# Kernel optimization log

Hardware: AMD Instinct MI355X
Metric: run time of the kernel (lower is better)

The kernel has to match this reference:

```python
import jax, jax.numpy as jnp
import numpy as np

THETA_BINS = 8
PHI_BINS = 8
BLOCK_SIZE = 15  # odd, per assert
STRIDE = 1       # with stride=1, nr_block along each axis == image dim
EPS = 2.220446049250313e-16  # sys.float_info.epsilon, as in the original


def setup_inputs() -> dict:
    key = jax.random.key(0)
    x = jax.random.normal(key, (96, 96, 96), dtype=jnp.float32)
    return {"x": x}


def _sliding_sum0(a, bs):
    """Sliding-window sum of size bs along axis 0, stride 1, nblocks = a.shape[0].
    Windows extending past the end see zeros (original code indexes past the image;
    we treat out-of-range voxels as zero contribution)."""
    pad = [(0, bs - 1)] + [(0, 0)] * (a.ndim - 1)
    cs = jnp.cumsum(jnp.pad(a, pad), axis=0)
    cs = jnp.concatenate([jnp.zeros_like(cs[:1]), cs], axis=0)  # exclusive prefix
    return cs[bs:] - cs[:-bs]  # out[i] = sum a[i:i+bs]


def reference(x):
    Z, Y, X = x.shape
    Tb, Pb, BS = THETA_BINS, PHI_BINS, BLOCK_SIZE
    B = Tb * Pb

    # conv3d with fixed central-difference kernels, padding=1 (zero pad)
    p = jnp.pad(x, 1)
    gz = p[2:, 1:-1, 1:-1] - p[:-2, 1:-1, 1:-1]
    gy = p[1:-1, 2:, 1:-1] - p[1:-1, :-2, 1:-1]
    gx = p[1:-1, 1:-1, 2:] - p[1:-1, 1:-1, :-2]

    r = jnp.sqrt(gx * gx + gy * gy + gz * gz)
    theta = jnp.arctan(gy / (gx + EPS))          # range (-pi/2, pi/2)
    phi = jnp.arccos(gz / (r + EPS))             # range [0, pi]

    two_pi = jnp.float32(2.0 * np.pi)
    theta = jnp.where(theta < 0, theta + two_pi, theta)  # angle_normalizer(theta,0,2pi)

    t_raw = theta / (two_pi / Tb)
    p_raw = phi / (jnp.float32(np.pi) / Pb)

    lt = jnp.floor(t_raw).astype(jnp.int32)
    lt = jnp.where(lt == Tb, 0, lt)
    lp = jnp.floor(p_raw).astype(jnp.int32)
    lp = jnp.where(lp == Pb, 0, lp)
    ht = (lt + 1) % Tb
    hp = (lp + 1) % Pb

    # NOTE: the original uses the THETA fractional part for the phi ratios too
    # (a bug in the source) - reproduced faithfully here.
    frac = t_raw - jnp.floor(t_raw)
    w_lo = jnp.minimum(frac, 1.0 - frac)   # low-bin ratio per the branchy original
    w_hi = 1.0 - w_lo                      # high-bin ratio
    wp_lo = jnp.where(frac == 0, jnp.float32(1.0), w_lo)  # frac==0 -> phi not split
    wp_hi = 1.0 - wp_lo

    # per-voxel soft-binned histogram volume [N, B] via 4 scatter-adds
    n = r.size
    rows = jnp.arange(n)
    rf = r.reshape(-1)
    ltf, htf = lt.reshape(-1), ht.reshape(-1)
    lpf, hpf = lp.reshape(-1), hp.reshape(-1)
    wlof, whif = w_lo.reshape(-1), w_hi.reshape(-1)
    wplof, wphif = wp_lo.reshape(-1), wp_hi.reshape(-1)

    V = jnp.zeros((n, B), dtype=r.dtype)
    V = V.at[rows, ltf * Pb + lpf].add(rf * wlof * wplof)
    V = V.at[rows, htf * Pb + lpf].add(rf * whif * wplof)
    V = V.at[rows, ltf * Pb + hpf].add(rf * wlof * wphif)
    V = V.at[rows, htf * Pb + hpf].add(rf * whif * wphif)
    V = V.reshape(Z, Y, X, B)

    # block histograms: separable sliding-window sum over block_size^3, stride 1
    for ax in (0, 1, 2):
        V = jnp.moveaxis(_sliding_sum0(jnp.moveaxis(V, ax, 0), BS), 0, ax)

    return V[None, None]  # [1, 1, nbz, nby, nbx, theta_bins*phi_bins]
```

## Files before the change

kernel.cpp:

```cpp
#include <hip/hip_runtime.h>

typedef _Float16 half_t;
typedef __attribute__((ext_vector_type(8))) _Float16 half8;
typedef __attribute__((ext_vector_type(4))) _Float16 half4;

#define DIM 96
#define NBINS 64
#define BSZ 15
#define PADROWS (DIM + BSZ - 1)
#define NTHREADS 256
#define RS_F 68
#define RS4_F 17
#define RS_H 72
#define TY 4
#define YTILES (DIM / TY)

__device__ __forceinline__ void bin_line_scatter(
    const float* __restrict__ in, float* __restrict__ V,
    const int y, const int z, const int tid, const float sgn)
{
    if (tid < DIM) {
        const int x = tid;
        const int idx = (z * DIM + y) * DIM + x;
        const float xm = (x > 0)       ? in[idx - 1]         : 0.0f;
        const float xp = (x < DIM - 1) ? in[idx + 1]         : 0.0f;
        const float ym = (y > 0)       ? in[idx - DIM]       : 0.0f;
        const float yp = (y < DIM - 1) ? in[idx + DIM]       : 0.0f;
        const float zm = (z > 0)       ? in[idx - DIM * DIM] : 0.0f;
        const float zp = (z < DIM - 1) ? in[idx + DIM * DIM] : 0.0f;
        const float gx = xp - xm, gy = yp - ym, gz = zp - zm;

        const float EPSF  = 2.220446049250313e-16f;
        const float TWOPI = 6.28318530717958647692f;
        const float PIF   = 3.14159265358979323846f;

        const float r = sqrtf(gx * gx + gy * gy + gz * gz);
        float theta = atanf(gy / (gx + EPSF));
        const float phi = acosf(gz / (r + EPSF));
        if (theta < 0.0f) theta += TWOPI;
        const float t_raw = theta / (TWOPI / 8.0f);
        const float p_raw = phi   / (PIF   / 8.0f);
        const float ft = floorf(t_raw);
        const float fp = floorf(p_raw);
        int lt = (int)ft; if (lt == 8) lt = 0;
        int lp = (int)fp; if (lp == 8) lp = 0;
        const int ht = (lt + 1) & 7;
        const int hp = (lp + 1) & 7;
        const float frac  = t_raw - ft;
        const float w_lo  = fminf(frac, 1.0f - frac);
        const float w_hi  = 1.0f - w_lo;
        const float wp_lo = (frac == 0.0f) ? 1.0f : w_lo;
        const float wp_hi = 1.0f - wp_lo;

        const float rs = r * sgn;
        float* vrow = V + x * RS_F;
        vrow[lt * 8 + lp] += rs * w_lo * wp_lo;
        vrow[ht * 8 + lp] += rs * w_hi * wp_lo;
        vrow[lt * 8 + hp] += rs * w_lo * wp_hi;
        vrow[ht * 8 + hp] += rs * w_hi * wp_hi;
    }
}

__global__ __launch_bounds__(NTHREADS) void kA_bin_xy_h(
    const float* __restrict__ in, half_t* __restrict__ ws1)
{
    __shared__ float V[PADROWS * RS_F];
    const int tid = threadIdx.x;
    const int y0 = blockIdx.x * TY;
    const int z  = blockIdx.y;

    for (int i = tid; i < PADROWS * RS4_F; i += NTHREADS)
        ((float4*)V)[i] = make_float4(0.f, 0.f, 0.f, 0.f);
    __syncthreads();

    #pragma unroll
    for (int j = 0; j < BSZ - 1; ++j) {
        const int ys = y0 + j;
        if (ys < DIM) bin_line_scatter(in, V, ys, z, tid, 1.0f);
    }

    const int c8 = tid & 7;
    const int strip = tid >> 3;
    const int pos0 = strip * 3;
    const float4* V4 = (const float4*)V;

    for (int r = 0; r < TY; ++r) {
        const int y = y0 + r;
        if (y + BSZ - 1 < DIM) bin_line_scatter(in, V, y + BSZ - 1, z, tid, 1.0f);
        __syncthreads();

        float acc[8];
        #pragma unroll
        for (int k = 0; k < 8; ++k) acc[k] = 0.f;
        #pragma unroll
        for (int d = 0; d < BSZ; ++d) {
            const float4 a = V4[(pos0 + d) * RS4_F + c8 * 2];
            const float4 b = V4[(pos0 + d) * RS4_F + c8 * 2 + 1];
            acc[0] += a.x; acc[1] += a.y; acc[2] += a.z; acc[3] += a.w;
            acc[4] += b.x; acc[5] += b.y; acc[6] += b.z; acc[7] += b.w;
        }
        int pos = pos0;
        #pragma unroll
        for (int j = 0; j < 3; ++j) {
            half8 o;
            #pragma unroll
            for (int k = 0; k < 8; ++k) o[k] = (half_t)acc[k];
            *(half8*)(ws1 + (((size_t)(z * DIM + y) * DIM + pos) * NBINS + c8 * 8)) = o;
            if (j < 2) {
                const float4 a0 = V4[pos * RS4_F + c8 * 2];
                const float4 b0 = V4[pos * RS4_F + c8 * 2 + 1];
                const float4 a1 = V4[(pos + BSZ) * RS4_F + c8 * 2];
                const float4 b1 = V4[(pos + BSZ) * RS4_F + c8 * 2 + 1];
                acc[0] += a1.x - a0.x; acc[1] += a1.y - a0.y;
                acc[2] += a1.z - a0.z; acc[3] += a1.w - a0.w;
                acc[4] += b1.x - b0.x; acc[5] += b1.y - b0.y;
                acc[6] += b1.z - b0.z; acc[7] += b1.w - b0.w;
                ++pos;
            }
        }
        __syncthreads();
        if (r < TY - 1)
            bin_line_scatter(in, V, y, z, tid, -1.0f);
    }
}

__global__ __launch_bounds__(NTHREADS) void k3_zsum_h(
    const half_t* __restrict__ ws2, float* __restrict__ out)
{
    __shared__ half_t H[PADROWS * RS_H];
    const int tid = threadIdx.x;
    const int x = blockIdx.x, y = blockIdx.y;

    for (int i = tid; i < DIM * 8; i += NTHREADS) {
        const int pos = i >> 3, c8 = i & 7;
        *(half8*)&H[pos * RS_H + c8 * 8] =
            *(const half8*)(ws2 + (((size_t)(pos * DIM + y) * DIM + x) * NBINS + c8 * 8));
    }
    for (int i = tid; i < (PADROWS - DIM) * 8; i += NTHREADS) {
        const int pos = DIM + (i >> 3), c8 = i & 7;
        half8 zv = {};
        *(half8*)&H[pos * RS_H + c8 * 8] = zv;
    }
    __syncthreads();

    const int c4 = tid & 15;
    const int strip = tid >> 4;
    int pos = strip * 6;

    float4 s = make_float4(0.f, 0.f, 0.f, 0.f);
    #pragma unroll
    for (int d = 0; d < BSZ; ++d) {
        const half4 hv = *(const half4*)&H[(pos + d) * RS_H + c4 * 4];
        s.x += (float)hv[0]; s.y += (float)hv[1];
        s.z += (float)hv[2]; s.w += (float)hv[3];
    }
    float4* out4 = (float4*)out;
    #pragma unroll
    for (int j = 0; j < 6; ++j) {
        out4[((size_t)(pos * DIM + y) * DIM + x) * 16 + c4] = s;
        if (j < 5) {
            const half4 hs = *(const half4*)&H[pos * RS_H + c4 * 4];
            const half4 ha = *(const half4*)&H[(pos + BSZ) * RS_H + c4 * 4];
            s.x += (float)ha[0] - (float)hs[0]; s.y += (float)ha[1] - (float)hs[1];
            s.z += (float)ha[2] - (float)hs[2]; s.w += (float)ha[3] - (float)hs[3];
            ++pos;
        }
    }
}

__global__ __launch_bounds__(NTHREADS) void k1_bin_xsum_f(
    const float* __restrict__ in, float* __restrict__ out)
{
    __shared__ float V[PADROWS * RS_F];
    const int tid = threadIdx.x;
    const int y = blockIdx.x, z = blockIdx.y;

    for (int i = tid; i < PADROWS * RS4_F; i += NTHREADS)
        ((float4*)V)[i] = make_float4(0.f, 0.f, 0.f, 0.f);
    __syncthreads();
    bin_line_scatter(in, V, y, z, tid, 1.0f);
    __syncthreads();

    const int c4 = tid & 15;
    const int strip = tid >> 4;
    int pos = strip * 6;
    const float4* V4 = (const float4*)V;

    float4 s = make_float4(0.f, 0.f, 0.f, 0.f);
    #pragma unroll
    for (int d = 0; d < BSZ; ++d) {
        const float4 v = V4[(pos + d) * RS4_F + c4];
        s.x += v.x; s.y += v.y; s.z += v.z; s.w += v.w;
    }
    float4* out4 = (float4*)out;
    const int base = (z * DIM + y) * DIM * 16;
    out4[base + pos * 16 + c4] = s;
    #pragma unroll
    for (int j = 1; j < 6; ++j) {
        const float4 a = V4[pos * RS4_F + c4];
        const float4 b = V4[(pos + BSZ) * RS4_F + c4];
        s.x += b.x - a.x; s.y += b.y - a.y; s.z += b.z - a.z; s.w += b.w - a.w;
        ++pos;
        out4[base + pos * 16 + c4] = s;
    }
}

__global__ __launch_bounds__(NTHREADS) void k_axis_sum_f(
    float* __restrict__ data, const int mulY, const int stride4)
{
    __shared__ float4 V4[PADROWS * RS4_F];
    const int tid = threadIdx.x;
    const int base4 = (blockIdx.y * mulY + blockIdx.x) * 16;
    float4* data4 = (float4*)data;

    for (int i = tid; i < DIM * 16; i += NTHREADS) {
        const int pos = i >> 4, c4 = i & 15;
        V4[pos * RS4_F + c4] = data4[base4 + (size_t)pos * stride4 + c4];
    }
    for (int i = tid; i < (PADROWS - DIM) * 16; i += NTHREADS) {
        const int pos = DIM + (i >> 4), c4 = i & 15;
        V4[pos * RS4_F + c4] = make_float4(0.f, 0.f, 0.f, 0.f);
    }
    __syncthreads();

    const int c4 = tid & 15;
    const int strip = tid >> 4;
    int pos = strip * 6;

    float4 s = make_float4(0.f, 0.f, 0.f, 0.f);
    #pragma unroll
    for (int d = 0; d < BSZ; ++d) {
        const float4 v = V4[(pos + d) * RS4_F + c4];
        s.x += v.x; s.y += v.y; s.z += v.z; s.w += v.w;
    }
    data4[base4 + (size_t)pos * stride4 + c4] = s;
    #pragma unroll
    for (int j = 1; j < 6; ++j) {
        const float4 a = V4[pos * RS4_F + c4];
        const float4 b = V4[(pos + BSZ) * RS4_F + c4];
        s.x += b.x - a.x; s.y += b.y - a.y; s.z += b.z - a.z; s.w += b.w - a.w;
        ++pos;
        data4[base4 + (size_t)pos * stride4 + c4] = s;
    }
}

extern "C" void kernel_launch(void* const* d_in, const int* in_sizes, int n_in,
                              void* d_out, int out_size, void* d_ws, size_t ws_size,
                              hipStream_t stream) {
    (void)in_sizes; (void)n_in; (void)out_size;
    const float* x = (const float*)d_in[0];
    float* out = (float*)d_out;
    const size_t nvox = (size_t)DIM * DIM * DIM * NBINS;
    const size_t need = nvox * sizeof(half_t);

    dim3 block(NTHREADS);
    if (ws_size >= need) {
        half_t* ws1 = (half_t*)d_ws;
        kA_bin_xy_h<<<dim3(YTILES, DIM), block, 0, stream>>>(x, ws1);
        k3_zsum_h<<<dim3(DIM, DIM), block, 0, stream>>>(ws1, out);
    } else {
        k1_bin_xsum_f<<<dim3(DIM, DIM), block, 0, stream>>>(x, out);
        k_axis_sum_f<<<dim3(DIM, DIM), block, 0, stream>>>(out, DIM * DIM * 16, DIM * 16);
        k_axis_sum_f<<<dim3(DIM, DIM), block, 0, stream>>>(out, DIM * 16, DIM * DIM * 16);
    }
}
```

Measured before the change: 326.9 us.

## Split binning into add/subtract LDS buffers and stream z-sum in registers

The xy-binning kernel now keeps two shared-memory histogram buffers. Half the threads scatter incoming rows into one buffer while the other half scatter departing rows with negative sign into the second, so both warp groups do useful scatter work. The y tile is doubled to 8 rows. The z-sum kernel is rewritten to process a full x-row per block, with each thread holding 24 bins in registers and sliding along 12 z slices, which removes the LDS staging and gives coalesced contiguous loads and stores. The cost is double LDS use (lower occupancy), two buffer reads in every window sum, and more halo rereads per z tile.

```diff
diff --git a/kernel.cpp b/kernel.cpp
--- a/kernel.cpp
+++ b/kernel.cpp
@@ -2,7 +2,6 @@
 
 typedef _Float16 half_t;
 typedef __attribute__((ext_vector_type(8))) _Float16 half8;
-typedef __attribute__((ext_vector_type(4))) _Float16 half4;
 
 #define DIM 96
 #define NBINS 64
@@ -11,16 +10,18 @@
 #define NTHREADS 256
 #define RS_F 68
 #define RS4_F 17
-#define RS_H 72
-#define TY 4
+#define TY 8
 #define YTILES (DIM / TY)
+#define TZ 12
+#define ZTILES (DIM / TZ)
+#define ROWE (DIM * NBINS)
+#define TPE 24
 
 __device__ __forceinline__ void bin_line_scatter(
     const float* __restrict__ in, float* __restrict__ V,
-    const int y, const int z, const int tid, const float sgn)
-{
-    if (tid < DIM) {
-        const int x = tid;
+    const int y, const int z, const int x, const float sgn)
+{
+    if (x < DIM) {
         const int idx = (z * DIM + y) * DIM + x;
         const float xm = (x > 0)       ? in[idx - 1]         : 0.0f;
         const float xp = (x < DIM - 1) ? in[idx + 1]         : 0.0f;
@@ -61,32 +62,44 @@
     }
 }
 
-__global__ __launch_bounds__(NTHREADS) void kA_bin_xy_h(
+__global__ __launch_bounds__(NTHREADS) void kA2_bin_xy_h(
     const float* __restrict__ in, half_t* __restrict__ ws1)
 {
-    __shared__ float V[PADROWS * RS_F];
+    __shared__ float A[PADROWS * RS_F];
+    __shared__ float B[PADROWS * RS_F];
     const int tid = threadIdx.x;
     const int y0 = blockIdx.x * TY;
     const int z  = blockIdx.y;
 
-    for (int i = tid; i < PADROWS * RS4_F; i += NTHREADS)
-        ((float4*)V)[i] = make_float4(0.f, 0.f, 0.f, 0.f);
+    for (int i = tid; i < PADROWS * RS4_F; i += NTHREADS) {
+        ((float4*)A)[i] = make_float4(0.f, 0.f, 0.f, 0.f);
+        ((float4*)B)[i] = make_float4(0.f, 0.f, 0.f, 0.f);
+    }
     __syncthreads();
 
-    #pragma unroll
-    for (int j = 0; j < BSZ - 1; ++j) {
-        const int ys = y0 + j;
-        if (ys < DIM) bin_line_scatter(in, V, ys, z, tid, 1.0f);
+    const int g = tid >> 7;
+    const int l = tid & 127;
+    float* P = g ? B : A;
+
+    #pragma unroll
+    for (int k = 0; k < (BSZ - 1) / 2; ++k) {
+        const int ys = y0 + 2 * k + g;
+        if (ys < DIM) bin_line_scatter(in, P, ys, z, l, 1.0f);
     }
 
     const int c8 = tid & 7;
     const int strip = tid >> 3;
     const int pos0 = strip * 3;
-    const float4* V4 = (const float4*)V;
+    const float4* A4 = (const float4*)A;
+    const float4* B4 = (const float4*)B;
 
     for (int r = 0; r < TY; ++r) {
         const int y = y0 + r;
-        if (y + BSZ - 1 < DIM) bin_line_scatter(in, V, y + BSZ - 1, z, tid, 1.0f);
+        if (g == 0) {
+            if (y + BSZ - 1 < DIM) bin_line_scatter(in, A, y + BSZ - 1, z, l, 1.0f);
+        } else {
+            if (r >= 1) bin_line_scatter(in, B, y - 1, z, l, -1.0f);
+        }
         __syncthreads();
 
         float acc[8];
@@ -94,10 +107,13 @@
         for (int k = 0; k < 8; ++k) acc[k] = 0.f;
         #pragma unroll
         for (int d = 0; d < BSZ; ++d) {
-            const float4 a = V4[(pos0 + d) * RS4_F + c8 * 2];
-            const float4 b = V4[(pos0 + d) * RS4_F + c8 * 2 + 1];
-            acc[0] += a.x; acc[1] += a.y; acc[2] += a.z; acc[3] += a.w;
-            acc[4] += b.x; acc[5] += b.y; acc[6] += b.z; acc[7] += b.w;
+            const int ri = (pos0 + d) * RS4_F + c8 * 2;
+            const float4 a  = A4[ri],     b  = A4[ri + 1];
+            const float4 a2 = B4[ri],     b2 = B4[ri + 1];
+            acc[0] += a.x + a2.x; acc[1] += a.y + a2.y;
+            acc[2] += a.z + a2.z; acc[3] += a.w + a2.w;
+            acc[4] += b.x + b2.x; acc[5] += b.y + b2.y;
+            acc[6] += b.z + b2.z; acc[7] += b.w + b2.w;
         }
         int pos = pos0;
         #pragma unroll
@@ -107,63 +123,85 @@
             for (int k = 0; k < 8; ++k) o[k] = (half_t)acc[k];
             *(half8*)(ws1 + (((size_t)(z * DIM + y) * DIM + pos) * NBINS + c8 * 8)) = o;
             if (j < 2) {
-                const float4 a0 = V4[pos * RS4_F + c8 * 2];
-                const float4 b0 = V4[pos * RS4_F + c8 * 2 + 1];
-                const float4 a1 = V4[(pos + BSZ) * RS4_F + c8 * 2];
-                const float4 b1 = V4[(pos + BSZ) * RS4_F + c8 * 2 + 1];
-                acc[0] += a1.x - a0.x; acc[1] += a1.y - a0.y;
-                acc[2] += a1.z - a0.z; acc[3] += a1.w - a0.w;
-                acc[4] += b1.x - b0.x; acc[5] += b1.y - b0.y;
-                acc[6] += b1.z - b0.z; acc[7] += b1.w - b0.w;
+                const int r0 = pos * RS4_F + c8 * 2;
+                const int r1 = (pos + BSZ) * RS4_F + c8 * 2;
+                const float4 a0 = A4[r0], b0 = A4[r0 + 1];
+                const float4 c0 = B4[r0], d0 = B4[r0 + 1];
+                const float4 a1 = A4[r1], b1 = A4[r1 + 1];
+                const float4 c1 = B4[r1], d1 = B4[r1 + 1];
+                acc[0] += (a1.x + c1.x) - (a0.x + c0.x);
+                acc[1] += (a1.y + c1.y) - (a0.y + c0.y);
+                acc[2] += (a1.z + c1.z) - (a0.z + c0.z);
+                acc[3] += (a1.w + c1.w) - (a0.w + c0.w);
+                acc[4] += (b1.x + d1.x) - (b0.x + d0.x);
+                acc[5] += (b1.y + d1.y) - (b0.y + d0.y);
+                acc[6] += (b1.z + d1.z) - (b0.z + d0.z);
+                acc[7] += (b1.w + d1.w) - (b0.w + d0.w);
                 ++pos;
             }
         }
         __syncthreads();
-        if (r < TY - 1)
-            bin_line_scatter(in, V, y, z, tid, -1.0f);
-    }
-}
-
-__global__ __launch_bounds__(NTHREADS) void k3_zsum_h(
-    const half_t* __restrict__ ws2, float* __restrict__ out)
-{
-    __shared__ half_t H[PADROWS * RS_H];
+    }
+}
+
+__global__ __launch_bounds__(NTHREADS) void k3_zstream_h(
+    const half_t* __restrict__ ws1, float* __restrict__ out)
+{
     const int tid = threadIdx.x;
-    const int x = blockIdx.x, y = blockIdx.y;
-
-    for (int i = tid; i < DIM * 8; i += NTHREADS) {
-        const int pos = i >> 3, c8 = i & 7;
-        *(half8*)&H[pos * RS_H + c8 * 8] =
-            *(const half8*)(ws2 + (((size_t)(pos * DIM + y) * DIM + x) * NBINS + c8 * 8));
-    }
-    for (int i = tid; i < (PADROWS - DIM) * 8; i += NTHREADS) {
-        const int pos = DIM + (i >> 3), c8 = i & 7;
-        half8 zv = {};
-        *(half8*)&H[pos * RS_H + c8 * 8] = zv;
-    }
-    __syncthreads();
-
-    const int c4 = tid & 15;
-    const int strip = tid >> 4;
-    int pos = strip * 6;
-
-    float4 s = make_float4(0.f, 0.f, 0.f, 0.f);
-    #pragma unroll
-    for (int d = 0; d < BSZ; ++d) {
-        const half4 hv = *(const half4*)&H[(pos + d) * RS_H + c4 * 4];
-        s.x += (float)hv[0]; s.y += (float)hv[1];
-        s.z += (float)hv[2]; s.w += (float)hv[3];
-    }
-    float4* out4 = (float4*)out;
-    #pragma unroll
-    for (int j = 0; j < 6; ++j) {
-        out4[((size_t)(pos * DIM + y) * DIM + x) * 16 + c4] = s;
-        if (j < 5) {
-            const half4 hs = *(const half4*)&H[pos * RS_H + c4 * 4];
-            const half4 ha = *(const half4*)&H[(pos + BSZ) * RS_H + c4 * 4];
-            s.x += (float)ha[0] - (float)hs[0]; s.y += (float)ha[1] - (float)hs[1];
-            s.z += (float)ha[2] - (float)hs[2]; s.w += (float)ha[3] - (float)hs[3];
-            ++pos;
+    const int y  = blockIdx.x;
+    const int z0 = blockIdx.y * TZ;
+    const int off = tid * TPE;
+
+    float acc[TPE];
+    #pragma unroll
+    for (int e = 0; e < TPE; ++e) acc[e] = 0.f;
+
+    #pragma unroll
+    for (int d = 0; d < BSZ - 1; ++d) {
+        const int zz = z0 + d;
+        if (zz < DIM) {
+            const half_t* p = ws1 + (size_t)(zz * DIM + y) * ROWE + off;
+            const half8 h0 = *(const half8*)(p);
+            const half8 h1 = *(const half8*)(p + 8);
+            const half8 h2 = *(const half8*)(p + 16);
+            #pragma unroll
+            for (int e = 0; e < 8; ++e) {
+                acc[e]      += (float)h0[e];
+                acc[8 + e]  += (float)h1[e];
+                acc[16 + e] += (float)h2[e];
+            }
+        }
+    }
+
+    for (int i = 0; i < TZ; ++i) {
+        const int z = z0 + i;
+        if (z + BSZ - 1 < DIM) {
+            const half_t* p = ws1 + (size_t)((z + BSZ - 1) * DIM + y) * ROWE + off;
+            const half8 h0 = *(const half8*)(p);
+            const half8 h1 = *(const half8*)(p + 8);
+            const half8 h2 = *(const half8*)(p + 16);
+            #pragma unroll
+            for (int e = 0; e < 8; ++e) {
+                acc[e]      += (float)h0[e];
+                acc[8 + e]  += (float)h1[e];
+                acc[16 + e] += (float)h2[e];
+            }
+        }
+        float4* op = (float4*)(out + (size_t)(z * DIM + y) * ROWE + off);
+        #pragma unroll
+        for (int q = 0; q < TPE / 4; ++q)
+            op[q] = make_float4(acc[4 * q], acc[4 * q + 1], acc[4 * q + 2], acc[4 * q + 3]);
+        if (i < TZ - 1) {
+            const half_t* p = ws1 + (size_t)(z * DIM + y) * ROWE + off;
+            const half8 h0 = *(const half8*)(p);
+            const half8 h1 = *(const half8*)(p + 8);
+            const half8 h2 = *(const half8*)(p + 16);
+            #pragma unroll
+            for (int e = 0; e < 8; ++e) {
+                acc[e]      -= (float)h0[e];
+                acc[8 + e]  -= (float)h1[e];
+                acc[16 + e] -= (float)h2[e];
+            }
         }
     }
 }
@@ -256,8 +294,8 @@
     dim3 block(NTHREADS);
     if (ws_size >= need) {
         half_t* ws1 = (half_t*)d_ws;
-        kA_bin_xy_h<<<dim3(YTILES, DIM), block, 0, stream>>>(x, ws1);
-        k3_zsum_h<<<dim3(DIM, DIM), block, 0, stream>>>(ws1, out);
+        kA2_bin_xy_h<<<dim3(YTILES, DIM), block, 0, stream>>>(x, ws1);
+        k3_zstream_h<<<dim3(DIM, ZTILES), block, 0, stream>>>(ws1, out);
     } else {
         k1_bin_xsum_f<<<dim3(DIM, DIM), block, 0, stream>>>(x, out);
         k_axis_sum_f<<<dim3(DIM, DIM), block, 0, stream>>>(out, DIM * DIM * 16, DIM * 16);
```

After: 387.4 us. +18.5%, slower.

## Replace per-column z-sum kernel with register-streaming z-tiled sliding sum

Applied to the files above, without the earlier changes.

The z-axis sliding-window kernel is rewritten so each block owns a full (y) row of X*bins elements and a tile of 12 z slices. Each thread keeps 24 running sums in registers and reads and writes contiguous rows, instead of loading one strided (x,y) column into shared memory per block. This removes the shared-memory staging and makes global accesses row-contiguous. In exchange, the 14-slice window halo is re-read for every z tile and there are fewer blocks (96x8).

```diff
diff --git a/kernel.cpp b/kernel.cpp
--- a/kernel.cpp
+++ b/kernel.cpp
@@ -2,7 +2,6 @@
 
 typedef _Float16 half_t;
 typedef __attribute__((ext_vector_type(8))) _Float16 half8;
-typedef __attribute__((ext_vector_type(4))) _Float16 half4;
 
 #define DIM 96
 #define NBINS 64
@@ -11,16 +10,17 @@
 #define NTHREADS 256
 #define RS_F 68
 #define RS4_F 17
-#define RS_H 72
 #define TY 4
 #define YTILES (DIM / TY)
+#define TZ 12
+#define ZTILES (DIM / TZ)
+#define ROWE (DIM * NBINS)
 
 __device__ __forceinline__ void bin_line_scatter(
     const float* __restrict__ in, float* __restrict__ V,
-    const int y, const int z, const int tid, const float sgn)
-{
-    if (tid < DIM) {
-        const int x = tid;
+    const int y, const int z, const int x, const float sgn)
+{
+    if (x < DIM) {
         const int idx = (z * DIM + y) * DIM + x;
         const float xm = (x > 0)       ? in[idx - 1]         : 0.0f;
         const float xp = (x < DIM - 1) ? in[idx + 1]         : 0.0f;
@@ -124,46 +124,60 @@
     }
 }
 
-__global__ __launch_bounds__(NTHREADS) void k3_zsum_h(
-    const half_t* __restrict__ ws2, float* __restrict__ out)
-{
-    __shared__ half_t H[PADROWS * RS_H];
-    const int tid = threadIdx.x;
-    const int x = blockIdx.x, y = blockIdx.y;
-
-    for (int i = tid; i < DIM * 8; i += NTHREADS) {
-        const int pos = i >> 3, c8 = i & 7;
-        *(half8*)&H[pos * RS_H + c8 * 8] =
-            *(const half8*)(ws2 + (((size_t)(pos * DIM + y) * DIM + x) * NBINS + c8 * 8));
-    }
-    for (int i = tid; i < (PADROWS - DIM) * 8; i += NTHREADS) {
-        const int pos = DIM + (i >> 3), c8 = i & 7;
-        half8 zv = {};
-        *(half8*)&H[pos * RS_H + c8 * 8] = zv;
-    }
-    __syncthreads();
-
-    const int c4 = tid & 15;
-    const int strip = tid >> 4;
-    int pos = strip * 6;
-
-    float4 s = make_float4(0.f, 0.f, 0.f, 0.f);
-    #pragma unroll
-    for (int d = 0; d < BSZ; ++d) {
-        const half4 hv = *(const half4*)&H[(pos + d) * RS_H + c4 * 4];
-        s.x += (float)hv[0]; s.y += (float)hv[1];
-        s.z += (float)hv[2]; s.w += (float)hv[3];
-    }
-    float4* out4 = (float4*)out;
-    #pragma unroll
-    for (int j = 0; j < 6; ++j) {
-        out4[((size_t)(pos * DIM + y) * DIM + x) * 16 + c4] = s;
-        if (j < 5) {
-            const half4 hs = *(const half4*)&H[pos * RS_H + c4 * 4];
-            const half4 ha = *(const half4*)&H[(pos + BSZ) * RS_H + c4 * 4];
-            s.x += (float)ha[0] - (float)hs[0]; s.y += (float)ha[1] - (float)hs[1];
-            s.z += (float)ha[2] - (float)hs[2]; s.w += (float)ha[3] - (float)hs[3];
-            ++pos;
+__global__ __launch_bounds__(NTHREADS) void k3_zstream_h(
+    const half_t* __restrict__ ws1, float* __restrict__ out)
+{
+    const int tid = threadIdx.x;
+    const int y  = blockIdx.x;
+    const int z0 = blockIdx.y * TZ;
+    const int e0 = tid * 8;
+
+    float acc[3][8];
+    #pragma unroll
+    for (int c = 0; c < 3; ++c)
+        #pragma unroll
+        for (int e = 0; e < 8; ++e) acc[c][e] = 0.f;
+
+    #pragma unroll
+    for (int d = 0; d < BSZ - 1; ++d) {
+        const int zz = z0 + d;
+        if (zz < DIM) {
+            const half_t* p = ws1 + (size_t)(zz * DIM + y) * ROWE + e0;
+            #pragma unroll
+            for (int c = 0; c < 3; ++c) {
+                const half8 h = *(const half8*)(p + c * 2048);
+                #pragma unroll
+                for (int e = 0; e < 8; ++e) acc[c][e] += (float)h[e];
+            }
+        }
+    }
+
+    for (int i = 0; i < TZ; ++i) {
+        const int z = z0 + i;
+        if (z + BSZ - 1 < DIM) {
+            const half_t* p = ws1 + (size_t)((z + BSZ - 1) * DIM + y) * ROWE + e0;
+            #pragma unroll
+            for (int c = 0; c < 3; ++c) {
+                const half8 h = *(const half8*)(p + c * 2048);
+                #pragma unroll
+                for (int e = 0; e < 8; ++e) acc[c][e] += (float)h[e];
+            }
+        }
+        float* op = out + (size_t)(z * DIM + y) * ROWE + e0;
+        #pragma unroll
+        for (int c = 0; c < 3; ++c) {
+            float4* o4 = (float4*)(op + c * 2048);
+            o4[0] = make_float4(acc[c][0], acc[c][1], acc[c][2], acc[c][3]);
+            o4[1] = make_float4(acc[c][4], acc[c][5], acc[c][6], acc[c][7]);
+        }
+        if (i < TZ - 1) {
+            const half_t* p = ws1 + (size_t)(z * DIM + y) * ROWE + e0;
+            #pragma unroll
+            for (int c = 0; c < 3; ++c) {
+                const half8 h = *(const half8*)(p + c * 2048);
+                #pragma unroll
+                for (int e = 0; e < 8; ++e) acc[c][e] -= (float)h[e];
+            }
         }
     }
 }
@@ -257,7 +271,7 @@
     if (ws_size >= need) {
         half_t* ws1 = (half_t*)d_ws;
         kA_bin_xy_h<<<dim3(YTILES, DIM), block, 0, stream>>>(x, ws1);
-        k3_zsum_h<<<dim3(DIM, DIM), block, 0, stream>>>(ws1, out);
+        k3_zstream_h<<<dim3(DIM, ZTILES), block, 0, stream>>>(ws1, out);
     } else {
         k1_bin_xsum_f<<<dim3(DIM, DIM), block, 0, stream>>>(x, out);
         k_axis_sum_f<<<dim3(DIM, DIM), block, 0, stream>>>(out, DIM * DIM * 16, DIM * 16);
```

New measurement: 341.7 us. 4.5% more time.
